# Kernel optimization log

Hardware: AMD Instinct MI355X
Metric: run time of the kernel (lower is better)

The kernel has to match this reference:

```python
import jax, jax.numpy as jnp
import numpy as np

B, S, D = 2, 2048, 2048
QH, KVH, HD = 32, 8, 64
GRP = QH // KVH  # GQA group size = 4


def setup_inputs() -> dict:
    key = jax.random.key(0)
    ks = jax.random.split(key, 9)
    x = jax.random.normal(ks[0], (B, S, D), jnp.float32)
    # RoPE angle table: [S, HD//2] -> stacked (cos, sin) -> [S, HD//2, 2]
    inv_freq = 1.0 / (10000.0 ** (np.arange(0, HD, 2, dtype=np.float32) / HD))
    ang = np.arange(S, dtype=np.float32)[:, None] * inv_freq[None, :]
    freqs = jnp.stack([jnp.cos(jnp.asarray(ang)), jnp.sin(jnp.asarray(ang))], axis=-1).astype(jnp.float32)
    w = 0.02
    Wq = jax.random.normal(ks[1], (D, QH * HD), jnp.float32) * w
    bq = jnp.zeros((QH * HD,), jnp.float32)
    Wk = jax.random.normal(ks[2], (D, KVH * HD), jnp.float32) * w
    bk = jnp.zeros((KVH * HD,), jnp.float32)
    Wv = jax.random.normal(ks[3], (D, KVH * HD), jnp.float32) * w
    bv = jnp.zeros((KVH * HD,), jnp.float32)
    Wo = jax.random.normal(ks[4], (QH * HD, D), jnp.float32) * w
    bo = jnp.zeros((D,), jnp.float32)
    return {"x": x, "freqs": freqs, "Wq": Wq, "bq": bq, "Wk": Wk, "bk": bk,
            "Wv": Wv, "bv": bv, "Wo": Wo, "bo": bo}


def _rope(xh, cos, sin):
    # xh: [b, s, h, hd]; complex rotation on adjacent pairs, like view_as_complex
    b, s, h, hd = xh.shape
    xp = xh.reshape(b, s, h, hd // 2, 2)
    x0, x1 = xp[..., 0], xp[..., 1]
    o0 = x0 * cos - x1 * sin
    o1 = x0 * sin + x1 * cos
    return jnp.stack([o0, o1], axis=-1).reshape(b, s, h, hd)


def reference(x, freqs, Wq, bq, Wk, bk, Wv, bv, Wo, bo):
    b, s, _ = x.shape
    q = (x @ Wq + bq).reshape(b, s, QH, HD)
    k = (x @ Wk + bk).reshape(b, s, KVH, HD)
    v = (x @ Wv + bv).reshape(b, s, KVH, HD)
    cos = freqs[:s, :, 0][None, :, None, :]  # [1, s, 1, hd//2]
    sin = freqs[:s, :, 1][None, :, None, :]
    q = _rope(q, cos, sin)
    k = _rope(k, cos, sin)
    # [b, h, s, hd]
    q = q.transpose(0, 2, 1, 3).reshape(b, KVH, GRP, s, HD)
    k = k.transpose(0, 2, 1, 3)  # [b, kvh, s, hd]
    v = v.transpose(0, 2, 1, 3)
    scores = jnp.einsum('bkgsh,bkth->bkgst', q, k) / jnp.sqrt(jnp.float32(HD))
    attn = jax.nn.softmax(scores, axis=-1)
    o = jnp.einsum('bkgst,bkth->bkgsh', attn, v)  # [b, kvh, grp, s, hd]
    o = o.reshape(b, QH, s, HD).transpose(0, 2, 1, 3).reshape(b, s, QH * HD)
    return o @ Wo + bo
```

## Files before the change

kernel.cpp:

```cpp
#include <hip/hip_runtime.h>
#include <stdint.h>

#define B_   2
#define S_   2048
#define D_   2048
#define QH_  32
#define KVH_ 8
#define HD_  64

typedef short  short8  __attribute__((ext_vector_type(8)));
typedef float  floatx4 __attribute__((ext_vector_type(4)));

__device__ __forceinline__ ushort f2b(float f) {
  union { float f; uint32_t u; } c; c.f = f;
  uint32_t u = c.u;
  return (ushort)((u + 0x7FFFu + ((u >> 16) & 1u)) >> 16);
}

__device__ __forceinline__ uint32_t fbits(float f) {
  union { float f; uint32_t u; } c; c.f = f;
  return c.u;
}

__device__ __forceinline__ short8 mk8(uint32_t a, uint32_t b, uint32_t c, uint32_t d) {
  union { uint4 u; short8 s; } v; v.u = (uint4){a, b, c, d}; return v.s;
}

__device__ __forceinline__ uint32_t cvtpk(float a, float b) {
  uint32_t r;
  asm("v_cvt_pk_bf16_f32 %0, %1, %2" : "=v"(r) : "v"(a), "v"(b));
  return r;
}

__device__ __forceinline__ void dma16(const void* g, void* l) {
  __builtin_amdgcn_global_load_lds(
      (const __attribute__((address_space(1))) uint32_t*)(uintptr_t)g,
      (__attribute__((address_space(3))) uint32_t*)(uintptr_t)l, 16, 0, 0);
}

#define QSCALE 0.18033688f


__global__ __launch_bounds__(256) void conv_x_kernel(const float* __restrict__ X,
                                                     ushort* __restrict__ Xb) {
  size_t i = ((size_t)blockIdx.x * 256 + threadIdx.x) * 4;
  float4 v = *(const float4*)(X + i);
  ushort4 o;
  o.x = f2b(v.x); o.y = f2b(v.y); o.z = f2b(v.z); o.w = f2b(v.w);
  *(ushort4*)(Xb + i) = o;
}

__global__ void tconv_all_kernel(const float* __restrict__ Wq, const float* __restrict__ Wk,
                                 const float* __restrict__ Wv, const float* __restrict__ Wo,
                                 ushort* __restrict__ wqkv, ushort* __restrict__ wo) {
  __shared__ float tile[32][33];
  int z = blockIdx.z;
  const float* W; ushort* Wt; int N;
  if (z == 0)      { W = Wq; Wt = wqkv;                        N = 2048; }
  else if (z == 1) { W = Wk; Wt = wqkv + (size_t)2048 * 2048;  N = 512;  }
  else if (z == 2) { W = Wv; Wt = wqkv + (size_t)2560 * 2048;  N = 512;  }
  else             { W = Wo; Wt = wo;                          N = 2048; }
  int bx = blockIdx.x, by = blockIdx.y;
  if (bx * 32 >= N) return;
  int tx = threadIdx.x, ty = threadIdx.y;
#pragma unroll
  for (int i = 0; i < 32; i += 8)
    tile[ty + i][tx] = W[(size_t)(by * 32 + ty + i) * N + bx * 32 + tx];
  __syncthreads();
#pragma unroll
  for (int i = 0; i < 32; i += 8)
    Wt[(size_t)(bx * 32 + ty + i) * 2048 + by * 32 + tx] = f2b(tile[tx][ty + i]);
}


__global__ __launch_bounds__(512, 2) void gemm_qkv_kernel(
    const ushort* __restrict__ A, const ushort* __restrict__ Bt,
    const float* __restrict__ bq, const float* __restrict__ bk,
    const float* __restrict__ bv, const float2* __restrict__ F2,
    ushort* __restrict__ qb, ushort* __restrict__ kb, ushort* __restrict__ vt) {
  __shared__ ushort sA[2][256 * 64];
  __shared__ ushort sB[2][256 * 64];
  const int tid  = threadIdx.x;
  const int bm   = blockIdx.y, bn = blockIdx.x;
  const int wave = tid >> 6, lane = tid & 63;
  const int quad = lane >> 4, l16 = lane & 15;
  const int wm2  = wave >> 2, wn4 = wave & 3;
  const int sw7  = l16 & 7;
  const int dr   = lane >> 3, du = (lane & 7) ^ dr;
  const int srow = wave * 8 + dr;
  const int lcol = (lane & 7) * 8;

  const ushort* Ab = A  + (size_t)(bm * 256) * 2048;
  const ushort* Bb = Bt + (size_t)(bn * 256) * 2048;

  floatx4 acc[8][4];
#pragma unroll
  for (int i = 0; i < 8; i++)
#pragma unroll
    for (int j = 0; j < 4; j++) acc[i][j] = (floatx4){0.f, 0.f, 0.f, 0.f};

  short8 af[4][2], bf[4][2];

#define STG_A(t, h) do {                                                      \
    dma16(Ab + (size_t)((h)*128 +      srow) * 2048 + (size_t)(t)*64 + du*8,  \
          &sA[(t)&1][((h)*128 +      srow) * 64 + lcol]);                     \
    dma16(Ab + (size_t)((h)*128 + 64 + srow) * 2048 + (size_t)(t)*64 + du*8,  \
          &sA[(t)&1][((h)*128 + 64 + srow) * 64 + lcol]);                     \
  } while (0)

#define STG_B(t, h) do {                                                      \
    dma16(Bb + (size_t)((h)*128 +      srow) * 2048 + (size_t)(t)*64 + du*8,  \
          &sB[(t)&1][((h)*128 +      srow) * 64 + lcol]);                     \
    dma16(Bb + (size_t)((h)*128 + 64 + srow) * 2048 + (size_t)(t)*64 + du*8,  \
          &sB[(t)&1][((h)*128 + 64 + srow) * 64 + lcol]);                     \
  } while (0)

#define LDA(Sb, mh) do {                                                      \
    _Pragma("unroll") for (int mi2 = 0; mi2 < 4; mi2++) {                     \
      const int rr = ((mh)*128 + wm2*64 + mi2*16 + l16) * 64;                 \
      af[mi2][0] = *(const short8*)&(Sb)[rr + (((quad    ) ^ sw7) * 8)];      \
      af[mi2][1] = *(const short8*)&(Sb)[rr + (((quad + 4) ^ sw7) * 8)];      \
    } } while (0)

#define LDB(Sb, nh) do {                                                      \
    _Pragma("unroll") for (int ni2 = 0; ni2 < 2; ni2++) {                     \
      const int rr = ((nh)*128 + wn4*32 + ni2*16 + l16) * 64;                 \
      bf[(nh)*2+ni2][0] = *(const short8*)&(Sb)[rr + (((quad    ) ^ sw7) * 8)]; \
      bf[(nh)*2+ni2][1] = *(const short8*)&(Sb)[rr + (((quad + 4) ^ sw7) * 8)]; \
    } } while (0)

#define MFMA_PH(mh, nh) do {                                                  \
    __builtin_amdgcn_s_setprio(1);                                           \
    _Pragma("unroll") for (int mi2 = 0; mi2 < 4; mi2++)                       \
    _Pragma("unroll") for (int ni2 = 0; ni2 < 2; ni2++)                       \
    _Pragma("unroll") for (int ks = 0; ks < 2; ks++)                          \
      acc[(mh)*4+mi2][(nh)*2+ni2] = __builtin_amdgcn_mfma_f32_16x16x32_bf16(  \
        af[mi2][ks], bf[(nh)*2+ni2][ks], acc[(mh)*4+mi2][(nh)*2+ni2], 0,0,0); \
    __builtin_amdgcn_s_setprio(0);                                            \
  } while (0)

#define PH_SYNC() do {                                                        \
    __builtin_amdgcn_sched_barrier(0);                                        \
    __builtin_amdgcn_s_barrier();                                             \
    asm volatile("s_waitcnt lgkmcnt(0)" ::: "memory");                        \
    __builtin_amdgcn_sched_barrier(0);                                        \
  } while (0)

#define PH_END() do {                                                         \
    __builtin_amdgcn_sched_barrier(0);                                        \
    __builtin_amdgcn_s_barrier();                                             \
    __builtin_amdgcn_sched_barrier(0);                                        \
  } while (0)

  STG_A(0, 0); STG_A(0, 1); STG_B(0, 0); STG_B(0, 1);
  STG_A(1, 0); STG_B(1, 0); STG_B(1, 1);
  asm volatile("s_waitcnt vmcnt(6)" ::: "memory");
  __builtin_amdgcn_s_barrier();

#pragma unroll 1
  for (int i = 0; i < 16; ++i) {
    const int t0 = 2 * i, t1 = 2 * i + 1;
    const bool more = (i < 15);
    const ushort* A0 = sA[0]; const ushort* B0 = sB[0];
    const ushort* A1 = sA[1]; const ushort* B1 = sB[1];

    LDB(B0, 0); LDA(A0, 0);
    STG_A(t1, 1);
    PH_SYNC(); MFMA_PH(0, 0); PH_END();

    LDB(B0, 1);
    if (more) STG_A(t0 + 2, 0);
    PH_SYNC(); MFMA_PH(0, 1); PH_END();

    LDA(A0, 1);
    if (more) STG_B(t0 + 2, 0);
    PH_SYNC(); MFMA_PH(1, 0); PH_END();

    if (more) STG_B(t0 + 2, 1);
    PH_SYNC(); MFMA_PH(1, 1);
    if (more) asm volatile("s_waitcnt vmcnt(6)" ::: "memory");
    else      asm volatile("s_waitcnt vmcnt(0)" ::: "memory");
    PH_END();

    LDB(B1, 0); LDA(A1, 0);
    if (more) STG_A(t0 + 2, 1);
    PH_SYNC(); MFMA_PH(0, 0); PH_END();

    LDB(B1, 1);
    if (more) STG_A(t1 + 2, 0);
    PH_SYNC(); MFMA_PH(0, 1); PH_END();

    LDA(A1, 1);
    if (more) STG_B(t1 + 2, 0);
    PH_SYNC(); MFMA_PH(1, 0); PH_END();

    if (more) STG_B(t1 + 2, 1);
    PH_SYNC(); MFMA_PH(1, 1);
    if (more) asm volatile("s_waitcnt vmcnt(6)" ::: "memory");
    PH_END();
  }

#undef STG_A
#undef STG_B
#undef LDA
#undef LDB
#undef MFMA_PH
#undef PH_SYNC
#undef PH_END

  const int isQ = (bn < 8);
  const int isV = (bn >= 10);
  const float sySign = (l16 & 1) ? 1.f : -1.f;

  const float* bsrc = isQ ? bq : (isV ? bv : bk);
  const int    boff = isQ ? 0  : (isV ? 2560 : 2048);

  float bvv[4];
#pragma unroll
  for (int ni = 0; ni < 4; ni++)
    bvv[ni] = bsrc[bn * 256 + (ni >> 1) * 128 + wn4 * 32 + (ni & 1) * 16 + l16 - boff];

  if (!isV) {
    ushort* dst = isQ ? qb : kb;
    const int NH   = isQ ? QH_ : KVH_;
    const int hoff = isQ ? 0 : 8;
    const int dpb  = l16 * 4 + (wn4 & 1) * 2;
#pragma unroll
    for (int mi = 0; mi < 8; mi++) {
#pragma unroll
      for (int r = 0; r < 4; r++) {
        int row = bm * 256 + (mi >> 2) * 128 + wm2 * 64 + (mi & 3) * 16 + quad * 4 + r;
        int s = row & 2047, bb = row >> 11;
        float o[4];
#pragma unroll
        for (int ni = 0; ni < 4; ni++) {
          float xv = acc[mi][ni][r] + bvv[ni];
          float2 cs = F2[s * 32 + (wn4 & 1) * 16 + (ni & 1) * 8 + (l16 >> 1)];
          float pp = __shfl_xor(xv, 1);
          float oo = fmaf(pp * sySign, cs.y, xv * cs.x);
          if (isQ) oo *= QSCALE;
          o[ni] = oo;
        }
#pragma unroll
        for (int hh = 0; hh < 2; hh++) {
          int h = (bn - hoff) * 4 + hh * 2 + (wn4 >> 1);
          size_t base = (((size_t)bb * NH + h) * S_ + s) * HD_ + dpb;
          ushort2 st; st.x = f2b(o[hh * 2 + 0]); st.y = f2b(o[hh * 2 + 1]);
          *(ushort2*)&dst[base] = st;
        }
      }
    }
  } else {
#pragma unroll
    for (int mi = 0; mi < 8; mi++) {
      int row0 = bm * 256 + (mi >> 2) * 128 + wm2 * 64 + (mi & 3) * 16 + quad * 4;
      int bb   = row0 >> 11;
      int posb = ((row0 & 2047) & ~63) + (mi & 2) * 16 + quad * 8 + (mi & 1) * 4;
#pragma unroll
      for (int ni = 0; ni < 4; ni++) {
        int h  = (bn - 10) * 4 + (ni >> 1) * 2 + (wn4 >> 1);
        int dt = (wn4 & 1) * 32 + (ni & 1) * 16 + l16;
        ushort4 st;
        st.x = f2b(acc[mi][ni][0] + bvv[ni]);
        st.y = f2b(acc[mi][ni][1] + bvv[ni]);
        st.z = f2b(acc[mi][ni][2] + bvv[ni]);
        st.w = f2b(acc[mi][ni][3] + bvv[ni]);
        *(ushort4*)&vt[(((size_t)bb * 8 + h) * 64 + dt) * (size_t)S_ + posb] = st;
      }
    }
  }
}


__global__ __launch_bounds__(256) void gemm_bt_kernel(
    const ushort* __restrict__ A, const ushort* __restrict__ Bt,
    const float* __restrict__ bias, float* __restrict__ C,
    int M, int N, int K) {
  __shared__ ushort sA[2][128 * 32];
  __shared__ ushort sB[2][128 * 32];
  const int tid  = threadIdx.x;
  const int bm   = blockIdx.y, bn = blockIdx.x;
  const int wave = tid >> 6, lane = tid & 63;
  const int quad = lane >> 4, l16 = lane & 15;
  const int wm   = (wave >> 1) * 64, wn = (wave & 1) * 64;

  const ushort* Ab = A  + (size_t)(bm * 128) * K;
  const ushort* Bb = Bt + (size_t)(bn * 128) * K;

  const int gr = lane >> 2;
  const int gu = (lane & 3) * 8;

  floatx4 acc[4][4];
#pragma unroll
  for (int i = 0; i < 4; i++)
#pragma unroll
    for (int j = 0; j < 4; j++) acc[i][j] = (floatx4){0.f, 0.f, 0.f, 0.f};

#pragma unroll
  for (int j = 0; j < 2; j++) {
    int row = j * 64 + wave * 16 + gr;
    dma16(Ab + (size_t)row * K + gu, &sA[0][j * 2048 + wave * 512]);
    dma16(Bb + (size_t)row * K + gu, &sB[0][j * 2048 + wave * 512]);
  }

  int cur = 0;
  for (int k0 = 0; k0 < K; k0 += 32) {
    __syncthreads();
    if (k0 + 32 < K) {
      int nxt = cur ^ 1;
#pragma unroll
      for (int j = 0; j < 2; j++) {
        int row = j * 64 + wave * 16 + gr;
        dma16(Ab + (size_t)row * K + k0 + 32 + gu, &sA[nxt][j * 2048 + wave * 512]);
        dma16(Bb + (size_t)row * K + k0 + 32 + gu, &sB[nxt][j * 2048 + wave * 512]);
      }
    }
    short8 af[4], bf[4];
#pragma unroll
    for (int mi = 0; mi < 4; mi++)
      af[mi] = *(const short8*)&sA[cur][(wm + mi * 16 + l16) * 32 + quad * 8];
#pragma unroll
    for (int ni = 0; ni < 4; ni++)
      bf[ni] = *(const short8*)&sB[cur][(wn + ni * 16 + l16) * 32 + quad * 8];
#pragma unroll
    for (int mi = 0; mi < 4; mi++)
#pragma unroll
      for (int ni = 0; ni < 4; ni++)
        acc[mi][ni] = __builtin_amdgcn_mfma_f32_16x16x32_bf16(
            af[mi], bf[ni], acc[mi][ni], 0, 0, 0);
    cur ^= 1;
  }

#pragma unroll
  for (int mi = 0; mi < 4; mi++) {
#pragma unroll
    for (int ni = 0; ni < 4; ni++) {
      int col  = bn * 128 + wn + ni * 16 + l16;
      float bv = bias[col];
#pragma unroll
      for (int r = 0; r < 4; r++) {
        int row = bm * 128 + wm + mi * 16 + quad * 4 + r;
        C[(size_t)row * N + col] = acc[mi][ni][r] + bv;
      }
    }
  }
}


__global__ __launch_bounds__(512, 4) void attn_kernel(
    const ushort* __restrict__ Q, const ushort* __restrict__ K,
    const ushort* __restrict__ Vt, ushort* __restrict__ O) {
  const int id  = blockIdx.x + 8 * (blockIdx.y + 32 * blockIdx.z);
  const int kvh = id & 7;
  const int qt  = (id >> 3) & 7;
  const int qh  = kvh * 4 + ((id >> 6) & 3);
  const int b   = id >> 8;
  const int tid = threadIdx.x;
  const int wave = tid >> 6, lane = tid & 63;
  const int quad = lane >> 4, l16 = lane & 15;

  __shared__ ushort kBuf[3][64 * 64];
  __shared__ ushort vBuf[3][64 * 64];

  const ushort* Qh = Q  + ((size_t)(b * QH_ + qh)) * S_ * HD_;
  const ushort* Kh = K  + ((size_t)(b * KVH_ + kvh)) * S_ * HD_;
  const ushort* Vh = Vt + ((size_t)(b * KVH_ + kvh)) * HD_ * S_;

  const int dr = lane >> 3;
  const int du = (lane & 7) ^ (dr & 7);
  const size_t kLaneOff = (size_t)(wave * 8 + dr) * 64 + du * 8;
  const size_t vLaneOff = (size_t)(wave * 8 + dr) * S_ + du * 8;
  const int swz = l16 & 7;

  const int q0 = qt * 256 + wave * 32;
  short8 aq[2][2];
#pragma unroll
  for (int m = 0; m < 2; m++)
#pragma unroll
    for (int s2 = 0; s2 < 2; s2++)
      aq[m][s2] = *(const short8*)(Qh + (size_t)(q0 + m * 16 + l16) * HD_ + s2 * 32 + quad * 8);

  floatx4 oacc[2][4];
#pragma unroll
  for (int m = 0; m < 2; m++)
#pragma unroll
    for (int t = 0; t < 4; t++) oacc[m][t] = (floatx4){0.f, 0.f, 0.f, 0.f};
  float ls[2] = {0.f, 0.f};

  dma16(Kh + kLaneOff, &kBuf[0][wave * 512]);
  dma16(Vh + vLaneOff, &vBuf[0][wave * 512]);
  dma16(Kh + (size_t)64 * 64 + kLaneOff, &kBuf[1][wave * 512]);
  dma16(Vh + 64 + vLaneOff,              &vBuf[1][wave * 512]);

#define ATTN_TILE(KB, VB)                                                     \
  do {                                                                        \
    _Pragma("unroll")                                                         \
    for (int u = 0; u < 2; u++) {                                             \
      uint32_t pk[2][4];                                                      \
      _Pragma("unroll")                                                       \
      for (int cc = 0; cc < 2; cc++) {                                        \
        const int c = u * 2 + cc;                                             \
        short8 kf0 = *(const short8*)&(KB)[(c * 16 + l16) * 64 + ((quad ^ swz) * 8)];        \
        short8 kf1 = *(const short8*)&(KB)[(c * 16 + l16) * 64 + (((4 + quad) ^ swz) * 8)];  \
        _Pragma("unroll")                                                     \
        for (int m = 0; m < 2; m++) {                                         \
          floatx4 sc = (floatx4){0.f, 0.f, 0.f, 0.f};                         \
          __builtin_amdgcn_s_setprio(1);                                      \
          sc = __builtin_amdgcn_mfma_f32_16x16x32_bf16(kf0, aq[m][0], sc, 0, 0, 0); \
          sc = __builtin_amdgcn_mfma_f32_16x16x32_bf16(kf1, aq[m][1], sc, 0, 0, 0); \
          __builtin_amdgcn_s_setprio(0);                                      \
          float p0 = __builtin_amdgcn_exp2f(sc[0]);                           \
          float p1 = __builtin_amdgcn_exp2f(sc[1]);                           \
          float p2 = __builtin_amdgcn_exp2f(sc[2]);                           \
          float p3 = __builtin_amdgcn_exp2f(sc[3]);                           \
          ls[m] += (p0 + p1) + (p2 + p3);                                     \
          pk[m][cc * 2 + 0] = cvtpk(p0, p1);                                  \
          pk[m][cc * 2 + 1] = cvtpk(p2, p3);                                  \
        }                                                                     \
      }                                                                       \
      _Pragma("unroll")                                                       \
      for (int t = 0; t < 4; t++) {                                           \
        const int row = (t * 16 + l16) * 64;                                  \
        short8 vf = *(const short8*)&(VB)[row + (((u * 4 + quad) ^ swz) * 8)]; \
        __builtin_amdgcn_s_setprio(1);                                        \
        _Pragma("unroll")                                                     \
        for (int m = 0; m < 2; m++) {                                         \
          short8 ap = mk8(pk[m][0], pk[m][1], pk[m][2], pk[m][3]);            \
          oacc[m][t] = __builtin_amdgcn_mfma_f32_16x16x32_bf16(ap, vf, oacc[m][t], 0, 0, 0); \
        }                                                                     \
        __builtin_amdgcn_s_setprio(0);                                        \
      }                                                                       \
    }                                                                         \
  } while (0)

  int cur = 0, stg = 2;
#pragma unroll 1
  for (int i = 0; i < 31; ++i) {
    __builtin_amdgcn_sched_barrier(0);
    asm volatile("s_waitcnt vmcnt(2)" ::: "memory");
    __builtin_amdgcn_s_barrier();
    __builtin_amdgcn_sched_barrier(0);

    if (i <= 29) {
      size_t kv2 = (size_t)(i + 2) * 64;
      dma16(Kh + kv2 * 64 + kLaneOff, &kBuf[stg][wave * 512]);
      dma16(Vh + kv2 + vLaneOff,      &vBuf[stg][wave * 512]);
      stg = (stg == 2) ? 0 : stg + 1;
    }

    ATTN_TILE(kBuf[cur], vBuf[cur]);
    cur = (cur == 2) ? 0 : cur + 1;
  }
  __builtin_amdgcn_sched_barrier(0);
  asm volatile("s_waitcnt vmcnt(0)" ::: "memory");
  __builtin_amdgcn_s_barrier();
  __builtin_amdgcn_sched_barrier(0);
  ATTN_TILE(kBuf[cur], vBuf[cur]);

#undef ATTN_TILE

#pragma unroll
  for (int m = 0; m < 2; m++) {
    ls[m] += __shfl_xor(ls[m], 16);
    ls[m] += __shfl_xor(ls[m], 32);
  }
#pragma unroll
  for (int m = 0; m < 2; m++) {
#pragma unroll
    for (int r = 0; r < 4; r++) {
      float l = __shfl(ls[m], (lane & 48) | (quad * 4 + r));
      float inv = 1.0f / l;
      int srow = q0 + m * 16 + quad * 4 + r;
      size_t base = ((size_t)b * S_ + srow) * (QH_ * HD_) + (size_t)qh * HD_;
#pragma unroll
      for (int t = 0; t < 4; t++)
        O[base + t * 16 + l16] = f2b(oacc[m][t][r] * inv);
    }
  }
}


extern "C" void kernel_launch(void* const* d_in, const int* in_sizes, int n_in,
                              void* d_out, int out_size, void* d_ws, size_t ws_size,
                              hipStream_t stream) {
  const float* x  = (const float*)d_in[0];
  const float* fr = (const float*)d_in[1];
  const float* Wq = (const float*)d_in[2];
  const float* bq = (const float*)d_in[3];
  const float* Wk = (const float*)d_in[4];
  const float* bk = (const float*)d_in[5];
  const float* Wv = (const float*)d_in[6];
  const float* bv = (const float*)d_in[7];
  const float* Wo = (const float*)d_in[8];
  const float* bo = (const float*)d_in[9];
  float* out = (float*)d_out;
  char* ws = (char*)d_ws;

  ushort* xb    = (ushort*)(ws + 0);
  ushort* wqkv  = (ushort*)(ws + 16777216);
  ushort* wo    = (ushort*)(ws + 29360128);
  ushort* qb    = (ushort*)(ws + 37761024);
  ushort* kb    = (ushort*)(ws + 54538240);
  ushort* vt    = (ushort*)(ws + 62926848);
  ushort* ob    = xb;

  conv_x_kernel<<<8192, 256, 0, stream>>>(x, xb);
  tconv_all_kernel<<<dim3(64, 64, 4), dim3(32, 8), 0, stream>>>(Wq, Wk, Wv, Wo, wqkv, wo);

  gemm_qkv_kernel<<<dim3(3072 / 256, 4096 / 256), 512, 0, stream>>>(
      xb, wqkv, bq, bk, bv, (const float2*)fr, qb, kb, vt);

  attn_kernel<<<dim3(8, 32, 2), 512, 0, stream>>>(qb, kb, vt, ob);

  gemm_bt_kernel<<<dim3(2048 / 128, 4096 / 128), 256, 0, stream>>>(
      ob, wo, bo, out, 4096, 2048, 2048);
}
```

Baseline: 302.6 us.

## Merge x conversion into weight prep kernel and compute softmax row sums via MFMA

The separate fp32-to-bf16 conversion of x is folded into the weight transpose/convert kernel as a fifth grid slice, so one launch replaces two. In attention, the per-lane scalar accumulation of exponentials plus the cross-lane shuffle reduction is replaced by an extra MFMA against a vector of bf16 ones, which gives each row's sum directly in the accumulator layout. This moves VALU adds and shuffles onto the matrix unit. The trade-off is one extra MFMA per tile step, and the row sum is now built from bf16-rounded probabilities rather than fp32 values.

```diff
diff --git a/kernel.cpp b/kernel.cpp
--- a/kernel.cpp
+++ b/kernel.cpp
@@ -41,20 +41,27 @@
 #define QSCALE 0.18033688f
 
 
-__global__ __launch_bounds__(256) void conv_x_kernel(const float* __restrict__ X,
-                                                     ushort* __restrict__ Xb) {
-  size_t i = ((size_t)blockIdx.x * 256 + threadIdx.x) * 4;
-  float4 v = *(const float4*)(X + i);
-  ushort4 o;
-  o.x = f2b(v.x); o.y = f2b(v.y); o.z = f2b(v.z); o.w = f2b(v.w);
-  *(ushort4*)(Xb + i) = o;
-}
-
-__global__ void tconv_all_kernel(const float* __restrict__ Wq, const float* __restrict__ Wk,
-                                 const float* __restrict__ Wv, const float* __restrict__ Wo,
-                                 ushort* __restrict__ wqkv, ushort* __restrict__ wo) {
+__global__ void prep_kernel(const float* __restrict__ Wq, const float* __restrict__ Wk,
+                            const float* __restrict__ Wv, const float* __restrict__ Wo,
+                            const float* __restrict__ X,
+                            ushort* __restrict__ wqkv, ushort* __restrict__ wo,
+                            ushort* __restrict__ Xb) {
   __shared__ float tile[32][33];
   int z = blockIdx.z;
+  int tx = threadIdx.x, ty = threadIdx.y;
+  if (z == 4) {
+    int bid = blockIdx.y * 64 + blockIdx.x;
+    int tid = ty * 32 + tx;
+    size_t i = ((size_t)bid * 256 + tid) * 8;
+    float4 v0 = *(const float4*)(X + i);
+    float4 v1 = *(const float4*)(X + i + 4);
+    ushort4 o0, o1;
+    o0.x = f2b(v0.x); o0.y = f2b(v0.y); o0.z = f2b(v0.z); o0.w = f2b(v0.w);
+    o1.x = f2b(v1.x); o1.y = f2b(v1.y); o1.z = f2b(v1.z); o1.w = f2b(v1.w);
+    *(ushort4*)(Xb + i)     = o0;
+    *(ushort4*)(Xb + i + 4) = o1;
+    return;
+  }
   const float* W; ushort* Wt; int N;
   if (z == 0)      { W = Wq; Wt = wqkv;                        N = 2048; }
   else if (z == 1) { W = Wk; Wt = wqkv + (size_t)2048 * 2048;  N = 512;  }
@@ -62,7 +69,6 @@
   else             { W = Wo; Wt = wo;                          N = 2048; }
   int bx = blockIdx.x, by = blockIdx.y;
   if (bx * 32 >= N) return;
-  int tx = threadIdx.x, ty = threadIdx.y;
 #pragma unroll
   for (int i = 0; i < 32; i += 8)
     tile[ty + i][tx] = W[(size_t)(by * 32 + ty + i) * N + bx * 32 + tx];
@@ -385,7 +391,10 @@
   for (int m = 0; m < 2; m++)
 #pragma unroll
     for (int t = 0; t < 4; t++) oacc[m][t] = (floatx4){0.f, 0.f, 0.f, 0.f};
-  float ls[2] = {0.f, 0.f};
+  floatx4 lsa[2];
+  lsa[0] = (floatx4){0.f, 0.f, 0.f, 0.f};
+  lsa[1] = (floatx4){0.f, 0.f, 0.f, 0.f};
+  const short8 vone = mk8(0x3F803F80u, 0x3F803F80u, 0x3F803F80u, 0x3F803F80u);
 
   dma16(Kh + kLaneOff, &kBuf[0][wave * 512]);
   dma16(Vh + vLaneOff, &vBuf[0][wave * 512]);
@@ -413,21 +422,21 @@
           float p1 = __builtin_amdgcn_exp2f(sc[1]);                           \
           float p2 = __builtin_amdgcn_exp2f(sc[2]);                           \
           float p3 = __builtin_amdgcn_exp2f(sc[3]);                           \
-          ls[m] += (p0 + p1) + (p2 + p3);                                     \
           pk[m][cc * 2 + 0] = cvtpk(p0, p1);                                  \
           pk[m][cc * 2 + 1] = cvtpk(p2, p3);                                  \
         }                                                                     \
       }                                                                       \
+      short8 ap0 = mk8(pk[0][0], pk[0][1], pk[0][2], pk[0][3]);               \
+      short8 ap1 = mk8(pk[1][0], pk[1][1], pk[1][2], pk[1][3]);               \
+      lsa[0] = __builtin_amdgcn_mfma_f32_16x16x32_bf16(ap0, vone, lsa[0], 0, 0, 0); \
+      lsa[1] = __builtin_amdgcn_mfma_f32_16x16x32_bf16(ap1, vone, lsa[1], 0, 0, 0); \
       _Pragma("unroll")                                                       \
       for (int t = 0; t < 4; t++) {                                           \
         const int row = (t * 16 + l16) * 64;                                  \
         short8 vf = *(const short8*)&(VB)[row + (((u * 4 + quad) ^ swz) * 8)]; \
         __builtin_amdgcn_s_setprio(1);                                        \
-        _Pragma("unroll")                                                     \
-        for (int m = 0; m < 2; m++) {                                         \
-          short8 ap = mk8(pk[m][0], pk[m][1], pk[m][2], pk[m][3]);            \
-          oacc[m][t] = __builtin_amdgcn_mfma_f32_16x16x32_bf16(ap, vf, oacc[m][t], 0, 0, 0); \
-        }                                                                     \
+        oacc[0][t] = __builtin_amdgcn_mfma_f32_16x16x32_bf16(ap0, vf, oacc[0][t], 0, 0, 0); \
+        oacc[1][t] = __builtin_amdgcn_mfma_f32_16x16x32_bf16(ap1, vf, oacc[1][t], 0, 0, 0); \
         __builtin_amdgcn_s_setprio(0);                                        \
       }                                                                       \
     }                                                                         \
@@ -461,15 +470,9 @@
 
 #pragma unroll
   for (int m = 0; m < 2; m++) {
-    ls[m] += __shfl_xor(ls[m], 16);
-    ls[m] += __shfl_xor(ls[m], 32);
-  }
-#pragma unroll
-  for (int m = 0; m < 2; m++) {
 #pragma unroll
     for (int r = 0; r < 4; r++) {
-      float l = __shfl(ls[m], (lane & 48) | (quad * 4 + r));
-      float inv = 1.0f / l;
+      float inv = 1.0f / lsa[m][r];
       int srow = q0 + m * 16 + quad * 4 + r;
       size_t base = ((size_t)b * S_ + srow) * (QH_ * HD_) + (size_t)qh * HD_;
 #pragma unroll
@@ -504,8 +507,8 @@
   ushort* vt    = (ushort*)(ws + 62926848);
   ushort* ob    = xb;
 
-  conv_x_kernel<<<8192, 256, 0, stream>>>(x, xb);
-  tconv_all_kernel<<<dim3(64, 64, 4), dim3(32, 8), 0, stream>>>(Wq, Wk, Wv, Wo, wqkv, wo);
+  prep_kernel<<<dim3(64, 64, 5), dim3(32, 8), 0, stream>>>(
+      Wq, Wk, Wv, Wo, x, wqkv, wo, xb);
 
   gemm_qkv_kernel<<<dim3(3072 / 256, 4096 / 256), 512, 0, stream>>>(
       xb, wqkv, bq, bk, bv, (const float2*)fr, qb, kb, vt);
```

New measurement: 291.8 us. 3.6% less time.
